# Kernel tuning notes

Measured on AMD Instinct MI355X. Metric: run time of the kernel, lower is better.

Reference implementation:

```python
import jax, jax.numpy as jnp
import numpy as np

BN_EPS = 1e-5


def _conv1x1(x, W, b):
    # x: (B, Cin, H, W), W: (Cout, Cin), b: (Cout,)
    return jnp.einsum('bchw,oc->bohw', x, W) + b[None, :, None, None]


def _bn(x, gamma, beta, mean, var):
    # inference-mode BatchNorm2d with running stats
    inv = gamma / jnp.sqrt(var + BN_EPS)
    return x * inv[None, :, None, None] + (beta - mean * inv)[None, :, None, None]


def setup_inputs() -> dict:
    key = jax.random.key(0)
    ks = jax.random.split(key, 8)
    B, N, C, H, W = 4, 3, 256, 48, 48
    Ck = C // 2  # key/query/value channels (scale=2)
    s = 0.02
    return {
        'x': jax.random.normal(ks[0], (B, N, C, H, W), jnp.float32),
        # f_key / f_query (shared): conv1x1 + BN
        'Wk': jax.random.normal(ks[1], (Ck, C), jnp.float32) * s,
        'bk': jnp.zeros((Ck,), jnp.float32),
        'gk': jnp.ones((Ck,), jnp.float32),
        'betak': jnp.zeros((Ck,), jnp.float32),
        'mk': jnp.zeros((Ck,), jnp.float32),
        'vk': jnp.ones((Ck,), jnp.float32),
        # f_value
        'Wv': jax.random.normal(ks[2], (Ck, C), jnp.float32) * s,
        'bv': jnp.zeros((Ck,), jnp.float32),
        # f_out
        'Wo': jax.random.normal(ks[3], (C, Ck), jnp.float32) * s,
        'bo': jnp.zeros((C,), jnp.float32),
        # fuse_layer: in = 2*C, out = C
        'Wf': jax.random.normal(ks[4], (C, 2 * C), jnp.float32) * s,
        'bf': jnp.zeros((C,), jnp.float32),
    }


def reference(x, Wk, bk, gk, betak, mk, vk, Wv, bv, Wo, bo, Wf, bf):
    B, N, C, H, W = x.shape  # N == 3
    HW = H * W
    Ck = Wk.shape[0]
    scale = Ck ** (-0.5)

    # Precompute shared key/query and value features for all 3 views
    xf = x.reshape(B * N, C, H, W)
    k_all = _bn(_conv1x1(xf, Wk, bk), gk, betak, mk, vk).reshape(B, N, Ck, HW)
    v_all = _conv1x1(xf, Wv, bv).reshape(B, N, Ck, HW)

    outs = []
    attn_maps = []
    for i in range(3):  # fixed small structural loop over views
        adj_ids = [j for j in range(3) if j != i]
        ref = x[:, i]                          # (B, C, H, W)
        q = k_all[:, i].transpose(0, 2, 1)     # (B, HW, Ck)  f_query == f_key
        matching = jnp.zeros_like(ref)
        for j in adj_ids:
            sim = jnp.einsum('bqc,bck->bqk', q, k_all[:, j]) * scale  # (B, HW, HW)
            attn = jax.nn.softmax(sim, axis=-1)
            ctx = jnp.einsum('bqk,bck->bcq', attn, v_all[:, j])       # (B, Ck, HW)
            ctx = ctx.reshape(B, Ck, H, W)
            matching = matching + _conv1x1(ctx, Wo, bo)
            if i == 0:
                attn_maps.append(attn)
        fuse = _conv1x1(jnp.concatenate([ref, matching], axis=1), Wf, bf)
        outs.append(ref + fuse)

    out = jnp.stack(outs, axis=1)                    # (B, 3, C, H, W)
    attention_maps = jnp.stack(attn_maps, axis=1)    # (B, 2, HW, HW)
    return out, attention_maps
```

## Files before the change

### kernel.cpp

```cpp
#include <hip/hip_runtime.h>

typedef short s8v __attribute__((ext_vector_type(8)));
typedef short s4v __attribute__((ext_vector_type(4)));
typedef float f4v __attribute__((ext_vector_type(4)));
typedef float f16v __attribute__((ext_vector_type(16)));
typedef unsigned u32v2 __attribute__((ext_vector_type(2)));
typedef unsigned u32v4 __attribute__((ext_vector_type(4)));
typedef unsigned short u16;

#define MFMA(a,b,c)   __builtin_amdgcn_mfma_f32_16x16x32_bf16(a,b,c,0,0,0)
#define MFMA32(a,b,c) __builtin_amdgcn_mfma_f32_32x32x16_bf16(a,b,c,0,0,0)

__device__ __forceinline__ float bf2f(u16 x){
  unsigned u = ((unsigned)x) << 16;
  return __builtin_bit_cast(float, u);
}
__device__ __forceinline__ u16 f2bf(float f){
  unsigned u = __builtin_bit_cast(unsigned, f);
  u += 0x7FFFu + ((u >> 16) & 1u);
  return (u16)(u >> 16);
}
__device__ __forceinline__ unsigned cvtpk(float lo, float hi){
  unsigned r;
  asm("v_cvt_pk_bf16_f32 %0, %1, %2" : "=v"(r) : "v"(lo), "v"(hi));
  return r;
}
__device__ __forceinline__ void plswap(unsigned &x, unsigned &y){
  asm volatile("v_permlane32_swap_b32 %0, %1" : "+v"(x), "+v"(y));
}

__device__ __forceinline__ void gload16(const void* g, void* l){
  __builtin_amdgcn_global_load_lds((const __attribute__((address_space(1))) unsigned*)g,
                                   (__attribute__((address_space(3))) unsigned*)l, 16, 0, 0);
}
__device__ __forceinline__ void nt_store4(float* p, f4v v){
  __builtin_nontemporal_store(v, (f4v*)p);
}

#define CC   256
#define CK   128
#define HW   2304
#define NF   12
#define C2E  0.1275174996992022f
#define OFF_KT   0u
#define OFF_V    7077888u
#define OFF_CTX  14155776u
#define OFF_RS   42467328u
#define OFF_PAR  42909696u
#define OFF_WK16 42911744u
#define OFF_WV16 42977280u
#define OFF_WF16 43042816u
#define OFF_WCMB 43304960u

__global__ void k0_params(const float* __restrict__ Wkf, const float* __restrict__ Wvf,
                          const float* __restrict__ bk, const float* __restrict__ gk,
                          const float* __restrict__ betak, const float* __restrict__ mk,
                          const float* __restrict__ vk, const float* __restrict__ Wo,
                          const float* __restrict__ Wf, const float* __restrict__ bo,
                          const float* __restrict__ bfv,
                          u16* __restrict__ Wk16, u16* __restrict__ Wv16, u16* __restrict__ Wf16,
                          float* kscale, float* kbias, float* btot, u16* Wcomb){
  int c = blockIdx.x;
  int o = threadIdx.x;
  int gid = c*256 + o;
  Wk16[gid] = f2bf(Wkf[gid]);
  Wv16[gid] = f2bf(Wvf[gid]);
  {
    f4v wf4 = *(const f4v*)(Wf + (size_t)gid*4);
    #pragma unroll
    for(int u=0;u<4;u++) Wf16[(size_t)gid*4+u] = f2bf(wf4[u]);
  }
  float acc = 0.f;
  for(int m=0;m<256;m++)
    acc += Wf[(size_t)o*512 + 256 + m] * Wo[(size_t)m*128 + c];
  Wcomb[(size_t)o*128 + c] = f2bf(acc);
  if (c == 0){
    float a2 = 0.f;
    for(int m=0;m<256;m++)
      a2 += Wf[(size_t)o*512 + 256 + m] * bo[m];
    btot[o] = bfv[o] + 2.0f*a2;
    if (o < 128){
      float inv = gk[o] * rsqrtf(vk[o] + 1e-5f);
      kscale[o] = inv;
      kbias[o]  = betak[o] + (bk[o] - mk[o])*inv;
    }
  }
}

__device__ __forceinline__ void stage_xt(const float* __restrict__ xf, int pb, int tid, char* xt){
  #pragma unroll
  for(int it=0; it<8; ++it){
    int idx = tid + 256*it;
    int cp = idx>>4, slot = idx&15;
    const float* s0 = xf + (size_t)(2*cp  )*HW + pb + slot*4;
    const float* s1 = xf + (size_t)(2*cp+1)*HW + pb + slot*4;
    f4v va = *(const f4v*)s0;
    f4v vb = *(const f4v*)s1;
    #pragma unroll
    for(int u=0;u<4;u++){
      int p = slot*4+u;
      *(unsigned*)(xt + p*512 + ((4*cp) ^ ((p&7)<<4))) = cvtpk(va[u], vb[u]);
    }
  }
}
__device__ __forceinline__ s8v xt_frag(const char* xt, int r, int kt, int g){
  return *(const s8v*)(xt + r*512 + (((unsigned)(64*kt+16*g)) ^ ((unsigned)(r&7)<<4)));
}

__global__ __launch_bounds__(256) void k1_kv(const float* __restrict__ x, const u16* __restrict__ Wk,
                                             const u16* __restrict__ Wv, const float* __restrict__ bv,
                                             const float* __restrict__ kscale, const float* __restrict__ kbias,
                                             u16* __restrict__ kT, u16* __restrict__ vout){
  int f  = blockIdx.y;
  int pb = blockIdx.x*64;
  int tid = threadIdx.x;
  int w = tid>>6, l = tid&63, s = l&15, g = l>>4;
  __shared__ char xt[32768];
  stage_xt(x + (size_t)f*CC*HW, pb, tid, xt);
  __syncthreads();
  {
    s8v afr[8];
    #pragma unroll
    for(int kt=0;kt<8;kt++) afr[kt] = xt_frag(xt, 16*w+s, kt, g);
    f4v acc[8] = {};
    #pragma unroll
    for(int kt=0;kt<8;kt++){
      #pragma unroll
      for(int nt=0;nt<8;nt++){
        s8v b = *(const s8v*)(Wk + (size_t)(16*nt+s)*CC + 32*kt + 8*g);
        acc[nt] = MFMA(afr[kt], b, acc[nt]);
      }
    }
    u16* kout = kT + (size_t)f*HW*CK;
    int q0 = pb + 16*w;
    #pragma unroll
    for(int nt=0;nt<8;nt++){
      int o = 16*nt + s;
      float sc = kscale[o], bi = kbias[o];
      #pragma unroll
      for(int r=0;r<4;r++){
        int q = q0 + 4*g + r;
        kout[(size_t)q*CK + o] = f2bf(acc[nt][r]*sc + bi);
      }
    }
  }
  {
    s8v afr[2][8];
    #pragma unroll
    for(int mt=0;mt<2;mt++)
      #pragma unroll
      for(int kt=0;kt<8;kt++)
        afr[mt][kt] = *(const s8v*)(Wv + (size_t)(32*w+16*mt+s)*CC + 32*kt + 8*g);
    f4v acc[2][4] = {};
    #pragma unroll
    for(int kt=0;kt<8;kt++){
      #pragma unroll
      for(int nt=0;nt<4;nt++){
        s8v b = xt_frag(xt, 16*nt+s, kt, g);
        #pragma unroll
        for(int mt=0;mt<2;mt++)
          acc[mt][nt] = MFMA(afr[mt][kt], b, acc[mt][nt]);
      }
    }
    u16* vf = vout + (size_t)f*CK*HW;
    #pragma unroll
    for(int mt=0;mt<2;mt++){
      #pragma unroll
      for(int r=0;r<4;r++){
        int o = 32*w + 16*mt + 4*g + r;
        float bvo = bv[o];
        #pragma unroll
        for(int nt=0;nt<4;nt++)
          vf[(size_t)o*HW + pb + 16*nt + s] = f2bf(acc[mt][nt][r] + bvo);
      }
    }
  }
}

__global__ __launch_bounds__(256, 2) void k2_attn(const u16* __restrict__ kT, const u16* __restrict__ v,
                                                  u16* __restrict__ ctxS, float* __restrict__ rs){
  int qb  = blockIdx.x;
  int yy  = blockIdx.y;
  int bij = yy>>1, half = yy&1;
  int b = bij/6, r6_ = bij - 6*b, i = r6_>>1, jj = r6_&1;
  int adj0 = (i==0) ? 1 : 0;
  int adj1 = (i==2) ? 1 : 2;
  int j = jj ? adj1 : adj0;
  int tid = threadIdx.x;
  int w = tid>>6, l = tid&63;
  int lq = l&31, hh = l>>5;
  int q0 = qb*128 + w*32;

  __shared__ char L[65536];

  const u16* kTi = kT + (size_t)(b*3+i)*HW*CK;
  const u16* kTj = kT + (size_t)(b*3+j)*HW*CK;
  const u16* vj  = v  + (size_t)(b*3+j)*CK*HW;

  s8v qfr[8];
  #pragma unroll
  for(int st=0; st<8; ++st)
    qfr[st] = *(const s8v*)(kTi + (size_t)(q0+lq)*CK + 16*st + 8*hh);

  f16v ctx[4] = {};
  float psum = 0.f;

  auto STAGE = [&](int p0, int buf){
    const char* kbase = (const char*)kTj + (size_t)p0*256;
    const char* vbase = (const char*)vj  + (size_t)p0*2;
    char* lK = L + buf*16384 + w*1024;
    char* lV = L + 32768 + buf*16384 + w*1024;
    #pragma unroll
    for(int it=0; it<4; ++it){
      unsigned Lo = (unsigned)tid*16u + (unsigned)it*4096u;
      unsigned Gs = Lo ^ (((Lo>>8)&7u)<<4);
      gload16(kbase + Gs, lK + it*4096);
      unsigned row = Lo>>7;
      unsigned col = (Lo & 127u) ^ ((row&7u)<<4);
      gload16(vbase + (size_t)row*(HW*2) + col, lV + it*4096);
    }
  };

  int pbase = half*18;
  STAGE(pbase*64, 0);
  __syncthreads();
  int cur = 0;

  for(int pt=0; pt<18; ++pt){
    int p0 = (pbase + pt)*64;
    if (pt < 17) STAGE(p0+64, cur^1);
    const char* lK = L + cur*16384;
    const char* lV = L + 32768 + cur*16384;

    f16v sa[2] = {};
    #pragma unroll
    for(int st=0; st<8; ++st){
      #pragma unroll
      for(int pb=0; pb<2; ++pb){
        unsigned row = (unsigned)(32*pb + lq);
        unsigned cb_ = ((unsigned)(32*st + 16*hh)) ^ ((row&7u)<<4);
        s8v kfr = *(const s8v*)(lK + row*256 + cb_);
        sa[pb] = MFMA32(kfr, qfr[st], sa[pb]);
      }
    }
    #pragma unroll
    for(int pb=0; pb<2; ++pb){
      float e0 = exp2f(sa[pb][0]*C2E),  e1 = exp2f(sa[pb][1]*C2E);
      float e2 = exp2f(sa[pb][2]*C2E),  e3 = exp2f(sa[pb][3]*C2E);
      float e4 = exp2f(sa[pb][4]*C2E),  e5 = exp2f(sa[pb][5]*C2E);
      float e6 = exp2f(sa[pb][6]*C2E),  e7 = exp2f(sa[pb][7]*C2E);
      float e8 = exp2f(sa[pb][8]*C2E),  e9 = exp2f(sa[pb][9]*C2E);
      float ea = exp2f(sa[pb][10]*C2E), eb = exp2f(sa[pb][11]*C2E);
      float ec = exp2f(sa[pb][12]*C2E), ed = exp2f(sa[pb][13]*C2E);
      float ee = exp2f(sa[pb][14]*C2E), ef = exp2f(sa[pb][15]*C2E);
      psum += ((e0+e1)+(e2+e3)) + ((e4+e5)+(e6+e7)) +
              ((e8+e9)+(ea+eb)) + ((ec+ed)+(ee+ef));
      unsigned c0 = cvtpk(e0,e1), c1 = cvtpk(e2,e3), c2 = cvtpk(e4,e5), c3 = cvtpk(e6,e7);
      unsigned c4 = cvtpk(e8,e9), c5 = cvtpk(ea,eb), c6 = cvtpk(ec,ed), c7 = cvtpk(ee,ef);
      plswap(c0, c2); plswap(c1, c3);
      plswap(c4, c6); plswap(c5, c7);
      u32v4 w0 = {c0, c1, c2, c3};
      u32v4 w1 = {c4, c5, c6, c7};
      s8v pf0 = __builtin_bit_cast(s8v, w0);
      s8v pf1 = __builtin_bit_cast(s8v, w1);
      #pragma unroll
      for(int cb=0; cb<4; ++cb){
        unsigned row = (unsigned)(32*cb + lq);
        unsigned swz = (row&7u)<<4;
        unsigned off0 = ((unsigned)(64*pb      + 16*hh)) ^ swz;
        unsigned off1 = ((unsigned)(64*pb + 32 + 16*hh)) ^ swz;
        s8v vf0 = *(const s8v*)(lV + row*128 + off0);
        s8v vf1 = *(const s8v*)(lV + row*128 + off1);
        ctx[cb] = MFMA32(vf0, pf0, ctx[cb]);
        ctx[cb] = MFMA32(vf1, pf1, ctx[cb]);
      }
    }
    __syncthreads();
    cur ^= 1;
  }

  float xsum = psum + __shfl_xor(psum, 32);
  if (l < 32)
    rs[(size_t)yy*HW + q0 + lq] = xsum;

  u16* cS = ctxS + (size_t)yy*HW*CK;
  #pragma unroll
  for(int cb=0; cb<4; ++cb){
    #pragma unroll
    for(int qd=0; qd<4; ++qd){
      u32v2 pk;
      pk[0] = cvtpk(ctx[cb][4*qd+0], ctx[cb][4*qd+1]);
      pk[1] = cvtpk(ctx[cb][4*qd+2], ctx[cb][4*qd+3]);
      *(u32v2*)(cS + (size_t)(q0+lq)*CK + 32*cb + 8*qd + 4*hh) = pk;
    }
  }
}

__global__ __launch_bounds__(256) void k2c_attnmap(const u16* __restrict__ kT,
                                                   const float* __restrict__ rs,
                                                   float* __restrict__ attn_out){
  int qb = blockIdx.x;
  int y  = blockIdx.y;
  int plane = y>>1, ph = y&1;
  int b = plane>>1, jj = plane&1, j = jj + 1;
  int tid = threadIdx.x;
  int w = tid>>6, l = tid&63, s = l&15, g = l>>4;
  int q0 = qb*64 + w*16;

  __shared__ char  ldsK[16384];
  __shared__ float ptile[4][16][68];
  __shared__ float inv16[4][16];

  const u16* kTi = kT + (size_t)(b*3)*HW*CK;
  const u16* kTj = kT + (size_t)(b*3+j)*HW*CK;

  s8v qf[4];
  #pragma unroll
  for(int kt=0;kt<4;kt++) qf[kt] = *(const s8v*)(kTi + (size_t)(q0+s)*CK + 32*kt + 8*g);

  {
    f4v ra = *(const f4v*)(rs + (size_t)(12*b+2*jj  )*HW + q0 + 4*g);
    f4v rb = *(const f4v*)(rs + (size_t)(12*b+2*jj+1)*HW + q0 + 4*g);
    if (s == 0){
      #pragma unroll
      for(int r=0;r<4;r++) inv16[w][4*g+r] = 1.0f / (ra[r] + rb[r]);
    }
  }
  __syncthreads();

  float* ao = attn_out + (size_t)plane*HW*HW;

  for(int pt=ph*18; pt<ph*18+18; ++pt){
    int p0 = pt*64;
    {
      const char* kbase = (const char*)kTj + (size_t)p0*256;
      char* lK = (char*)ldsK + w*1024;
      #pragma unroll
      for(int it=0; it<4; ++it){
        unsigned Lo = (unsigned)tid*16u + (unsigned)it*4096u;
        unsigned Gs = Lo ^ (((Lo>>8)&7u)<<4);
        gload16(kbase + Gs, lK + it*4096);
      }
    }
    __syncthreads();

    f4v sa[4] = {};
    #pragma unroll
    for(int kt=0;kt<4;kt++){
      #pragma unroll
      for(int nt=0;nt<4;nt++){
        unsigned row = (unsigned)(16*nt + s);
        unsigned cb  = ((unsigned)(64*kt + 16*g)) ^ ((row&7u)<<4);
        s8v bfr = *(const s8v*)((const char*)ldsK + row*256 + cb);
        sa[nt] = MFMA(qf[kt], bfr, sa[nt]);
      }
    }
    #pragma unroll
    for(int r=0;r<4;r++){
      #pragma unroll
      for(int nt=0;nt<4;nt++)
        ptile[w][4*g+r][16*nt+s] = exp2f(sa[nt][r]*C2E);
    }
    #pragma unroll
    for(int pass=0; pass<4; ++pass){
      int row = 4*pass + g;
      float inv = inv16[w][row];
      f4v val = *(const f4v*)&ptile[w][row][4*s];
      #pragma unroll
      for(int u=0;u<4;u++) val[u] *= inv;
      nt_store4(ao + (size_t)(q0+row)*HW + p0 + 4*s, val);
    }
    __syncthreads();
  }
}

__global__ __launch_bounds__(256) void k3_out(const float* __restrict__ x,
                                              const u16* __restrict__ Wf, const u16* __restrict__ Wcomb,
                                              const float* __restrict__ btot, const u16* __restrict__ ctxS,
                                              const float* __restrict__ rs,
                                              float* __restrict__ out){
  int f = blockIdx.y, pb = blockIdx.x*64;
  int tid = threadIdx.x;
  int w = tid>>6, l = tid&63, s = l&15, g = l>>4;
  __shared__ char xt[32768];
  const float* xf = x + (size_t)f*CC*HW;
  stage_xt(xf, pb, tid, xt);
  __syncthreads();
  f4v acc[4][4] = {};
  #pragma unroll
  for(int kt=0;kt<8;kt++){
    s8v bfr[4];
    #pragma unroll
    for(int nt=0;nt<4;nt++) bfr[nt] = xt_frag(xt, 16*nt+s, kt, g);
    #pragma unroll
    for(int mt=0;mt<4;mt++){
      s8v a = *(const s8v*)(Wf + (size_t)(64*w+16*mt+s)*512 + 32*kt + 8*g);
      #pragma unroll
      for(int nt=0;nt<4;nt++) acc[mt][nt] = MFMA(a, bfr[nt], acc[mt][nt]);
    }
  }
  #pragma unroll
  for(int jj=0;jj<2;jj++){
    const u16* cA = ctxS + (size_t)(4*f+2*jj  )*HW*CK;
    const u16* cB = ctxS + (size_t)(4*f+2*jj+1)*HW*CK;
    f4v acc2[4][4] = {};
    #pragma unroll
    for(int kt=0;kt<4;kt++){
      s8v b0[4], b1[4];
      #pragma unroll
      for(int nt=0;nt<4;nt++){
        b0[nt] = *(const s8v*)(cA + (size_t)(pb+16*nt+s)*CK + 32*kt + 8*g);
        b1[nt] = *(const s8v*)(cB + (size_t)(pb+16*nt+s)*CK + 32*kt + 8*g);
      }
      #pragma unroll
      for(int mt=0;mt<4;mt++){
        s8v a = *(const s8v*)(Wcomb + (size_t)(64*w+16*mt+s)*CK + 32*kt + 8*g);
        #pragma unroll
        for(int nt=0;nt<4;nt++){
          acc2[mt][nt] = MFMA(a, b0[nt], acc2[mt][nt]);
          acc2[mt][nt] = MFMA(a, b1[nt], acc2[mt][nt]);
        }
      }
    }
    const float* rA = rs + (size_t)(4*f+2*jj  )*HW;
    const float* rB = rs + (size_t)(4*f+2*jj+1)*HW;
    float invq[4];
    #pragma unroll
    for(int nt=0;nt<4;nt++){
      int q = pb + 16*nt + s;
      invq[nt] = 1.0f / (rA[q] + rB[q]);
    }
    #pragma unroll
    for(int mt=0;mt<4;mt++)
      #pragma unroll
      for(int nt=0;nt<4;nt++)
        #pragma unroll
        for(int r=0;r<4;r++) acc[mt][nt][r] += acc2[mt][nt][r]*invq[nt];
  }
  float* of = out + (size_t)f*CC*HW;
  #pragma unroll
  for(int mt=0;mt<4;mt++){
    #pragma unroll
    for(int r=0;r<4;r++){
      int o = 64*w + 16*mt + 4*g + r;
      float bb = btot[o];
      #pragma unroll
      for(int nt=0;nt<4;nt++){
        int p = pb + 16*nt + s;
        of[(size_t)o*HW + p] = acc[mt][nt][r] + bb + xf[(size_t)o*HW + p];
      }
    }
  }
}

extern "C" void kernel_launch(void* const* d_in, const int* in_sizes, int n_in,
                              void* d_out, int out_size, void* d_ws, size_t ws_size,
                              hipStream_t stream) {
  const float* x     = (const float*)d_in[0];
  const float* Wk    = (const float*)d_in[1];
  const float* bk    = (const float*)d_in[2];
  const float* gk    = (const float*)d_in[3];
  const float* betak = (const float*)d_in[4];
  const float* mk    = (const float*)d_in[5];
  const float* vk    = (const float*)d_in[6];
  const float* Wv    = (const float*)d_in[7];
  const float* bv    = (const float*)d_in[8];
  const float* Wo    = (const float*)d_in[9];
  const float* bo    = (const float*)d_in[10];
  const float* Wf    = (const float*)d_in[11];
  const float* bf    = (const float*)d_in[12];
  float* out = (float*)d_out;

  char* ws = (char*)d_ws;
  u16*   kT     = (u16*)(ws + OFF_KT);
  u16*   vv     = (u16*)(ws + OFF_V);
  u16*   ctxS   = (u16*)(ws + OFF_CTX);
  float* rs     = (float*)(ws + OFF_RS);
  float* kscale = (float*)(ws + OFF_PAR);
  float* kbias  = kscale + 128;
  float* btot   = kbias + 128;
  u16*   Wk16   = (u16*)(ws + OFF_WK16);
  u16*   Wv16   = (u16*)(ws + OFF_WV16);
  u16*   Wf16   = (u16*)(ws + OFF_WF16);
  u16*   Wcomb  = (u16*)(ws + OFF_WCMB);

  float* attn = out + (size_t)NF*CC*HW;

  k0_params<<<dim3(128), dim3(256), 0, stream>>>(Wk, Wv, bk, gk, betak, mk, vk, Wo, Wf, bo, bf,
                                                 Wk16, Wv16, Wf16, kscale, kbias, btot, Wcomb);
  k1_kv<<<dim3(36,12), dim3(256), 0, stream>>>(x, Wk16, Wv16, bv, kscale, kbias, kT, vv);
  k2_attn<<<dim3(18,48), dim3(256), 0, stream>>>(kT, vv, ctxS, rs);
  k2c_attnmap<<<dim3(36,16), dim3(256), 0, stream>>>(kT, rs, attn);
  k3_out<<<dim3(36,12), dim3(256), 0, stream>>>(x, Wf16, Wcomb, btot, ctxS, rs, out);
}
```

Before: 218.6 us.

## Single-buffer V tile in attention kernel to fit three blocks per CU

The attention kernel keeps the K tile double-buffered but stages V into a single LDS buffer, cutting shared memory from 64KB to 48KB and raising launch bounds to three blocks per CU. V loads for the next tile are issued after the PV MFMAs, with explicit vmcnt waits and barriers so the K prefetch and the V refill overlap correctly. The aim is more resident waves to hide latency, at the cost of an extra barrier per iteration, exposed V-load latency, and tighter register limits.

```diff
diff --git a/kernel.cpp b/kernel.cpp
--- a/kernel.cpp
+++ b/kernel.cpp
@@ -177,7 +177,7 @@
   }
 }
 
-__global__ __launch_bounds__(256, 2) void k2_attn(const u16* __restrict__ kT, const u16* __restrict__ v,
+__global__ __launch_bounds__(256, 3) void k2_attn(const u16* __restrict__ kT, const u16* __restrict__ v,
                                                   u16* __restrict__ ctxS, float* __restrict__ rs){
   int qb  = blockIdx.x;
   int yy  = blockIdx.y;
@@ -191,7 +191,7 @@
   int lq = l&31, hh = l>>5;
   int q0 = qb*128 + w*32;
 
-  __shared__ char L[65536];
+  __shared__ char L[49152];
 
   const u16* kTi = kT + (size_t)(b*3+i)*HW*CK;
   const u16* kTj = kT + (size_t)(b*3+j)*HW*CK;
@@ -205,16 +205,22 @@
   f16v ctx[4] = {};
   float psum = 0.f;
 
-  auto STAGE = [&](int p0, int buf){
+  auto STAGE_K = [&](int p0, int buf){
     const char* kbase = (const char*)kTj + (size_t)p0*256;
-    const char* vbase = (const char*)vj  + (size_t)p0*2;
     char* lK = L + buf*16384 + w*1024;
-    char* lV = L + 32768 + buf*16384 + w*1024;
     #pragma unroll
     for(int it=0; it<4; ++it){
       unsigned Lo = (unsigned)tid*16u + (unsigned)it*4096u;
       unsigned Gs = Lo ^ (((Lo>>8)&7u)<<4);
       gload16(kbase + Gs, lK + it*4096);
+    }
+  };
+  auto STAGE_V = [&](int p0){
+    const char* vbase = (const char*)vj + (size_t)p0*2;
+    char* lV = L + 32768 + w*1024;
+    #pragma unroll
+    for(int it=0; it<4; ++it){
+      unsigned Lo = (unsigned)tid*16u + (unsigned)it*4096u;
       unsigned row = Lo>>7;
       unsigned col = (Lo & 127u) ^ ((row&7u)<<4);
       gload16(vbase + (size_t)row*(HW*2) + col, lV + it*4096);
@@ -222,15 +228,16 @@
   };
 
   int pbase = half*18;
-  STAGE(pbase*64, 0);
+  STAGE_K(pbase*64, 0);
+  STAGE_V(pbase*64);
   __syncthreads();
-  int cur = 0;
+  int kcur = 0;
 
   for(int pt=0; pt<18; ++pt){
     int p0 = (pbase + pt)*64;
-    if (pt < 17) STAGE(p0+64, cur^1);
-    const char* lK = L + cur*16384;
-    const char* lV = L + 32768 + cur*16384;
+    if (pt < 17) STAGE_K(p0+64, kcur^1);
+    const char* lK = L + kcur*16384;
+    const char* lV = L + 32768;
 
     f16v sa[2] = {};
     #pragma unroll
@@ -243,6 +250,7 @@
         sa[pb] = MFMA32(kfr, qfr[st], sa[pb]);
       }
     }
+    s8v pf[2][2];
     #pragma unroll
     for(int pb=0; pb<2; ++pb){
       float e0 = exp2f(sa[pb][0]*C2E),  e1 = exp2f(sa[pb][1]*C2E);
@@ -261,8 +269,15 @@
       plswap(c4, c6); plswap(c5, c7);
       u32v4 w0 = {c0, c1, c2, c3};
       u32v4 w1 = {c4, c5, c6, c7};
-      s8v pf0 = __builtin_bit_cast(s8v, w0);
-      s8v pf1 = __builtin_bit_cast(s8v, w1);
+      pf[pb][0] = __builtin_bit_cast(s8v, w0);
+      pf[pb][1] = __builtin_bit_cast(s8v, w1);
+    }
+    if (pt < 17) asm volatile("s_waitcnt vmcnt(4)" ::: "memory");
+    else         asm volatile("s_waitcnt vmcnt(0)" ::: "memory");
+    __builtin_amdgcn_s_barrier();
+    __builtin_amdgcn_sched_barrier(0);
+    #pragma unroll
+    for(int pb=0; pb<2; ++pb){
       #pragma unroll
       for(int cb=0; cb<4; ++cb){
         unsigned row = (unsigned)(32*cb + lq);
@@ -271,12 +286,20 @@
         unsigned off1 = ((unsigned)(64*pb + 32 + 16*hh)) ^ swz;
         s8v vf0 = *(const s8v*)(lV + row*128 + off0);
         s8v vf1 = *(const s8v*)(lV + row*128 + off1);
-        ctx[cb] = MFMA32(vf0, pf0, ctx[cb]);
-        ctx[cb] = MFMA32(vf1, pf1, ctx[cb]);
-      }
-    }
-    __syncthreads();
-    cur ^= 1;
+        ctx[cb] = MFMA32(vf0, pf[pb][0], ctx[cb]);
+        ctx[cb] = MFMA32(vf1, pf[pb][1], ctx[cb]);
+      }
+    }
+    asm volatile("s_waitcnt lgkmcnt(0)" ::: "memory");
+    __builtin_amdgcn_s_barrier();
+    __builtin_amdgcn_sched_barrier(0);
+    if (pt < 17){
+      STAGE_V(p0+64);
+      asm volatile("s_waitcnt vmcnt(4)" ::: "memory");
+      __builtin_amdgcn_s_barrier();
+      __builtin_amdgcn_sched_barrier(0);
+    }
+    kcur ^= 1;
   }
 
   float xsum = psum + __shfl_xor(psum, 32);
```

New measurement: 226.4 us. 1.04x slower.
